# Optimization experiments

Hardware: AMD Instinct MI355X
Metric: run time of the kernel (lower is better)

The kernel has to match this reference:

```python
import jax, jax.numpy as jnp
import numpy as np


def setup_inputs() -> dict:
    key = jax.random.key(0)
    k1, k2, k3 = jax.random.split(key, 3)
    B, L, C, K = 8, 4096, 1024, 7
    x = jax.random.normal(k1, (B, L, C), dtype=jnp.float32)
    # torch Conv1d(groups=channels) weight: [C, 1, K], bias: [C]
    weight = jax.random.normal(k2, (C, 1, K), dtype=jnp.float32) * 0.1
    bias = jax.random.normal(k3, (C,), dtype=jnp.float32) * 0.1
    return {"x": x, "weight": weight, "bias": bias}


def reference(x, weight, bias):
    # x: [B, L, C]; weight: [C, 1, K]; bias: [C]
    C = weight.shape[0]
    K = weight.shape[2]
    xt = jnp.transpose(x, (0, 2, 1))  # [B, C, L]
    # causal pad (K-1 on the left) fused into conv padding
    y = jax.lax.conv_general_dilated(
        xt,
        weight,
        window_strides=(1,),
        padding=[(K - 1, 0)],
        dimension_numbers=("NCH", "OIH", "NCH"),
        feature_group_count=C,
    )  # [B, C, L]
    y = y + bias[None, :, None]
    return jnp.transpose(y, (0, 2, 1))  # [B, L, C]
```

## Files before the change

### kernel.cpp

```cpp
#include <hip/hip_runtime.h>


constexpr int Lc  = 4096;
constexpr int C4  = 256;
constexpr int K   = 7;
constexpr int LT  = 16;

__global__ __launch_bounds__(256) void dwconv_kernel(
    const float4* __restrict__ x, const float* __restrict__ w,
    const float* __restrict__ bias, float4* __restrict__ y) {
  const int c4 = threadIdx.x;
  const int l0 = blockIdx.x * LT;
  const int b  = blockIdx.y;
  const int c  = c4 * 4;

  float wk[K][4];
#pragma unroll
  for (int k = 0; k < K; ++k) {
#pragma unroll
    for (int j = 0; j < 4; ++j) {
      wk[k][j] = w[(c + j) * K + k];
    }
  }

  float4 bv;
  bv.x = bias[c + 0];
  bv.y = bias[c + 1];
  bv.z = bias[c + 2];
  bv.w = bias[c + 3];

  const float4* xb = x + (size_t)b * Lc * C4 + c4;
  float4*       yb = y + (size_t)b * Lc * C4 + c4;

  float4 win[K];
#pragma unroll
  for (int i = 0; i < K - 1; ++i) {
    const int l = l0 - (K - 1) + i;
    if (l >= 0) {
      win[i] = xb[(size_t)l * C4];
    } else {
      win[i] = make_float4(0.f, 0.f, 0.f, 0.f);
    }
  }

#pragma unroll
  for (int i = 0; i < LT; ++i) {
    const int l = l0 + i;
    win[(i + K - 1) % K] = xb[(size_t)l * C4];
    float4 acc = bv;
#pragma unroll
    for (int k = 0; k < K; ++k) {
      const float4 v = win[(i + k) % K];
      acc.x = fmaf(wk[k][0], v.x, acc.x);
      acc.y = fmaf(wk[k][1], v.y, acc.y);
      acc.z = fmaf(wk[k][2], v.z, acc.z);
      acc.w = fmaf(wk[k][3], v.w, acc.w);
    }
    yb[(size_t)l * C4] = acc;
  }
}

extern "C" void kernel_launch(void* const* d_in, const int* in_sizes, int n_in,
                              void* d_out, int out_size, void* d_ws, size_t ws_size,
                              hipStream_t stream) {
  const float4* x    = (const float4*)d_in[0];
  const float*  w    = (const float*)d_in[1];
  const float*  bias = (const float*)d_in[2];
  float4*       y    = (float4*)d_out;

  const int B = 8;
  dim3 grid(Lc / LT, B, 1);
  dim3 block(C4, 1, 1);
  dwconv_kernel<<<grid, block, 0, stream>>>(x, w, bias, y);
}
```

Measured before the change: 52.42 us.

## Vectorize weight loads, double tile length, prefetch rows, use nontemporal stores

Raises the per-block sequence tile from 16 to 32 rows, which halves the redundant halo reads. Weights and bias are now loaded as contiguous float4 vectors instead of strided scalars. The input rows are held in a register array and loaded two 4-row groups ahead of the compute. The grid tile index is swizzled across blocks, and outputs are written with nontemporal stores to avoid polluting the cache. The larger register array and the launch-bounds occupancy hint could cost occupancy or cause register spills.

```diff
diff --git a/kernel.cpp b/kernel.cpp
--- a/kernel.cpp
+++ b/kernel.cpp
@@ -1,72 +1,83 @@
 #include <hip/hip_runtime.h>
 
 
-constexpr int Lc  = 4096;
-constexpr int C4  = 256;
-constexpr int K   = 7;
-constexpr int LT  = 16;
+typedef float f32x4 __attribute__((ext_vector_type(4)));
 
-__global__ __launch_bounds__(256) void dwconv_kernel(
-    const float4* __restrict__ x, const float* __restrict__ w,
-    const float* __restrict__ bias, float4* __restrict__ y) {
+constexpr int Lc = 4096;
+constexpr int C4 = 256;
+constexpr int K  = 7;
+constexpr int LT = 32;
+constexpr int NB = LT / 4;
+
+__global__ __launch_bounds__(256, 4) void dwconv_kernel(
+    const f32x4* __restrict__ x, const float* __restrict__ w,
+    const float* __restrict__ bias, f32x4* __restrict__ y) {
   const int c4 = threadIdx.x;
-  const int l0 = blockIdx.x * LT;
+  const int bx = blockIdx.x;
+  const int tile = ((bx & 7) << 4) | (bx >> 3);
+  const int l0 = tile * LT;
   const int b  = blockIdx.y;
   const int c  = c4 * 4;
 
-  float wk[K][4];
+  float ww[28];
+  {
+    const f32x4* wv = reinterpret_cast<const f32x4*>(w + (size_t)c * K);
 #pragma unroll
-  for (int k = 0; k < K; ++k) {
-#pragma unroll
-    for (int j = 0; j < 4; ++j) {
-      wk[k][j] = w[(c + j) * K + k];
+    for (int i = 0; i < 7; ++i) {
+      f32x4 t = wv[i];
+      ww[i * 4 + 0] = t.x; ww[i * 4 + 1] = t.y;
+      ww[i * 4 + 2] = t.z; ww[i * 4 + 3] = t.w;
     }
   }
+  const f32x4 bv = reinterpret_cast<const f32x4*>(bias)[c4];
 
-  float4 bv;
-  bv.x = bias[c + 0];
-  bv.y = bias[c + 1];
-  bv.z = bias[c + 2];
-  bv.w = bias[c + 3];
+  const f32x4* xb = x + (size_t)b * Lc * C4 + c4;
+  f32x4*       yb = y + (size_t)b * Lc * C4 + c4;
 
-  const float4* xb = x + (size_t)b * Lc * C4 + c4;
-  float4*       yb = y + (size_t)b * Lc * C4 + c4;
-
-  float4 win[K];
+  f32x4 v[LT + 6];
+  const f32x4 fz = {0.f, 0.f, 0.f, 0.f};
 #pragma unroll
-  for (int i = 0; i < K - 1; ++i) {
-    const int l = l0 - (K - 1) + i;
-    if (l >= 0) {
-      win[i] = xb[(size_t)l * C4];
-    } else {
-      win[i] = make_float4(0.f, 0.f, 0.f, 0.f);
-    }
+  for (int i = 0; i < 6; ++i) {
+    const int l = l0 - 6 + i;
+    v[i] = (l >= 0) ? xb[(size_t)l * C4] : fz;
+  }
+#pragma unroll
+  for (int i = 0; i < 8; ++i) {
+    v[6 + i] = xb[(size_t)(l0 + i) * C4];
   }
 
 #pragma unroll
-  for (int i = 0; i < LT; ++i) {
-    const int l = l0 + i;
-    win[(i + K - 1) % K] = xb[(size_t)l * C4];
-    float4 acc = bv;
+  for (int jb = 0; jb < NB; ++jb) {
+    if (jb + 2 < NB) {
 #pragma unroll
-    for (int k = 0; k < K; ++k) {
-      const float4 v = win[(i + k) % K];
-      acc.x = fmaf(wk[k][0], v.x, acc.x);
-      acc.y = fmaf(wk[k][1], v.y, acc.y);
-      acc.z = fmaf(wk[k][2], v.z, acc.z);
-      acc.w = fmaf(wk[k][3], v.w, acc.w);
+      for (int i = 0; i < 4; ++i) {
+        v[6 + (jb + 2) * 4 + i] = xb[(size_t)(l0 + (jb + 2) * 4 + i) * C4];
+      }
     }
-    yb[(size_t)l * C4] = acc;
+#pragma unroll
+    for (int i = 0; i < 4; ++i) {
+      const int li = jb * 4 + i;
+      f32x4 acc = bv;
+#pragma unroll
+      for (int k = 0; k < K; ++k) {
+        const f32x4 xv = v[li + k];
+        acc.x = fmaf(ww[0 * 7 + k], xv.x, acc.x);
+        acc.y = fmaf(ww[1 * 7 + k], xv.y, acc.y);
+        acc.z = fmaf(ww[2 * 7 + k], xv.z, acc.z);
+        acc.w = fmaf(ww[3 * 7 + k], xv.w, acc.w);
+      }
+      __builtin_nontemporal_store(acc, &yb[(size_t)(l0 + li) * C4]);
+    }
   }
 }
 
 extern "C" void kernel_launch(void* const* d_in, const int* in_sizes, int n_in,
                               void* d_out, int out_size, void* d_ws, size_t ws_size,
                               hipStream_t stream) {
-  const float4* x    = (const float4*)d_in[0];
-  const float*  w    = (const float*)d_in[1];
-  const float*  bias = (const float*)d_in[2];
-  float4*       y    = (float4*)d_out;
+  const f32x4* x    = (const f32x4*)d_in[0];
+  const float* w    = (const float*)d_in[1];
+  const float* bias = (const float*)d_in[2];
+  f32x4*       y    = (f32x4*)d_out;
 
   const int B = 8;
   dim3 grid(Lc / LT, B, 1);
```

Result: faster. 47.43 us (-9.5%).
